# Optimization experiments

Hardware: AMD Instinct MI355X
Metric: run time of the kernel (lower is better)

Reference implementation:

```python
import jax, jax.numpy as jnp
import numpy as np

N = 8192
IN_F = 512
OUT_F = 256
ALPHA = 0.2          # LeakyReLU negative slope
MASK_VAL = -9e15     # same sentinel as the torch code


def setup_inputs() -> dict:
    key = jax.random.key(0)
    k1, k2, k3, k4, k5, k6 = jax.random.split(key, 6)
    inputs = jax.random.normal(k1, (N, IN_F), dtype=jnp.float32)
    # sparse-ish 0/1 dense adjacency (~avg degree 64)
    adj = (jax.random.uniform(k2, (N, N)) < (64.0 / N)).astype(jnp.float32)
    W = jax.random.normal(k3, (IN_F, OUT_F), dtype=jnp.float32) * (1.414 / np.sqrt(IN_F))
    a = jax.random.normal(k4, (2 * OUT_F, 1), dtype=jnp.float32) * 0.1
    W_gc = jax.random.normal(k5, (IN_F, OUT_F), dtype=jnp.float32) * (1.414 / np.sqrt(IN_F))
    b_gc = jax.random.normal(k6, (OUT_F,), dtype=jnp.float32) * 0.01
    return {"inputs": inputs, "adj": adj, "W": W, "a": a, "W_gc": W_gc, "b_gc": b_gc}


def reference(inputs, adj, W, a, W_gc, b_gc):
    # h: [n, F]
    h = inputs @ W
    F = h.shape[1]
    # Fused additive attention: e[i,j] = leaky_relu(a1.h_i + a2.h_j)
    # (mathematically identical to the repeat/cat construction in the source)
    f_src = h @ a[:F, 0]   # [n]
    f_dst = h @ a[F:, 0]   # [n]
    e = jax.nn.leaky_relu(f_src[:, None] + f_dst[None, :], negative_slope=ALPHA)  # [n, n]
    # masked row-softmax over neighbors
    att = jnp.where(adj > 0, e, MASK_VAL)
    att = jax.nn.softmax(att, axis=1)
    # dropout p=0.0 -> identity
    h_prime = att @ h  # [n, F]
    # optional dense graph-convolution branch (graph_convolve=True)
    gc = adj @ (inputs @ W_gc) + b_gc
    return h_prime + gc
```

## Files before the change

kernel.cpp:

```cpp
#include <hip/hip_runtime.h>
#include <hip/hip_bf16.h>
#include <math.h>

#define N_NODES 8192
#define IN_F    512
#define OUT_F   256
#define NCAT    512
#define ALPHA   0.2f
#define MAXDEG  512

typedef __attribute__((ext_vector_type(8))) short short8;
typedef __attribute__((ext_vector_type(4))) float f32x4;

static __device__ __forceinline__ short f2bf(float f) {
    union { float f; unsigned u; } v; v.f = f;
    unsigned r = v.u + 0x7fffu + ((v.u >> 16) & 1u);
    return (short)(r >> 16);
}
static __device__ __forceinline__ float bf2f(short s) {
    union { unsigned u; float f; } v;
    v.u = ((unsigned)(unsigned short)s) << 16;
    return v.f;
}

__global__ __launch_bounds__(512) void bt_pack(const float* __restrict__ W,
                                               const float* __restrict__ W_gc,
                                               short* __restrict__ Bt) {
    const int n = blockIdx.x;
    const int k = threadIdx.x;
    const int c = n >> 1;
    float v = (n & 1) ? W_gc[(size_t)k * OUT_F + c] : W[(size_t)k * OUT_F + c];
    Bt[(size_t)n * IN_F + k] = f2bf(v);
}

__global__ __launch_bounds__(256) void gemm_mfma(const float* __restrict__ A,
                                                 const short* __restrict__ Bt,
                                                 short* __restrict__ hcat) {
    __shared__ short As[128 * 32];
    __shared__ short Bs[128 * 32];

    const int tid  = threadIdx.x;
    const int m0   = blockIdx.y * 128;
    const int n0   = blockIdx.x * 128;
    const int wid  = tid >> 6;
    const int lane = tid & 63;
    const int wr   = wid >> 1;
    const int wc   = wid & 1;
    const int mh   = lane & 15;
    const int q    = lane >> 4;

    const int srow  = tid >> 1;
    const int shalf = tid & 1;

    const f32x4 vzero = {0.f, 0.f, 0.f, 0.f};
    f32x4 acc[4][4];
    #pragma unroll
    for (int i = 0; i < 4; i++)
        #pragma unroll
        for (int j = 0; j < 4; j++) acc[i][j] = vzero;

    const float* aga = A  + (size_t)(m0 + srow) * IN_F + shalf * 16;
    const short* bgb = Bt + (size_t)(n0 + srow) * IN_F + shalf * 16;
    short* asw = &As[srow * 32 + shalf * 16];
    short* bsw = &Bs[srow * 32 + shalf * 16];

    for (int k0 = 0; k0 < IN_F; k0 += 32) {
        const float4* a4 = (const float4*)(aga + k0);
        float4 x0 = a4[0], x1 = a4[1], x2 = a4[2], x3 = a4[3];
        const int4* b4 = (const int4*)(bgb + k0);
        int4 bv0 = b4[0], bv1 = b4[1];

        short8 p0, p1;
        p0[0] = f2bf(x0.x); p0[1] = f2bf(x0.y); p0[2] = f2bf(x0.z); p0[3] = f2bf(x0.w);
        p0[4] = f2bf(x1.x); p0[5] = f2bf(x1.y); p0[6] = f2bf(x1.z); p0[7] = f2bf(x1.w);
        p1[0] = f2bf(x2.x); p1[1] = f2bf(x2.y); p1[2] = f2bf(x2.z); p1[3] = f2bf(x2.w);
        p1[4] = f2bf(x3.x); p1[5] = f2bf(x3.y); p1[6] = f2bf(x3.z); p1[7] = f2bf(x3.w);

        __syncthreads();
        *(short8*)asw       = p0;
        *(short8*)(asw + 8) = p1;
        *(int4*)bsw         = bv0;
        *(int4*)(bsw + 8)   = bv1;
        __syncthreads();

        short8 af[4], bfm[4];
        #pragma unroll
        for (int i = 0; i < 4; i++) {
            af[i]  = *(const short8*)&As[(wr * 64 + i * 16 + mh) * 32 + q * 8];
            bfm[i] = *(const short8*)&Bs[(wc * 64 + i * 16 + mh) * 32 + q * 8];
        }
        #pragma unroll
        for (int mi = 0; mi < 4; mi++)
            #pragma unroll
            for (int ni = 0; ni < 4; ni++)
                acc[mi][ni] = __builtin_amdgcn_mfma_f32_16x16x32_bf16(
                    af[mi], bfm[ni], acc[mi][ni], 0, 0, 0);
    }

    #pragma unroll
    for (int mi = 0; mi < 4; mi++)
        #pragma unroll
        for (int ni = 0; ni < 4; ni++) {
            const int col   = n0 + wc * 64 + ni * 16 + mh;
            const int rbase = m0 + wr * 64 + mi * 16 + q * 4;
            f32x4 v = acc[mi][ni];
            #pragma unroll
            for (int r = 0; r < 4; r++)
                hcat[(size_t)(rbase + r) * NCAT + col] = f2bf(v[r]);
        }
}

__global__ __launch_bounds__(256) void compute_f(const short* __restrict__ hcat,
                                                 const float* __restrict__ a,
                                                 float* __restrict__ f_src,
                                                 float* __restrict__ f_dst) {
    const int row  = blockIdx.x * 4 + (threadIdx.x >> 6);
    const int lane = threadIdx.x & 63;
    const short* hr = hcat + (size_t)row * NCAT;
    float s1 = 0.f, s2 = 0.f;
    #pragma unroll
    for (int c = lane; c < OUT_F; c += 64) {
        float hv = bf2f(hr[2 * c]);
        s1 += hv * a[c];
        s2 += hv * a[OUT_F + c];
    }
    #pragma unroll
    for (int off = 32; off; off >>= 1) {
        s1 += __shfl_down(s1, off);
        s2 += __shfl_down(s2, off);
    }
    if (lane == 0) { f_src[row] = s1; f_dst[row] = s2; }
}

__global__ __launch_bounds__(256) void attn_row(const float* __restrict__ adj,
                                                const short* __restrict__ hcat,
                                                const float* __restrict__ f_src,
                                                const float* __restrict__ f_dst,
                                                const float* __restrict__ b_gc,
                                                float* __restrict__ out) {
    __shared__ int   s_idx[MAXDEG];
    __shared__ float s_w[MAXDEG];
    __shared__ float s_red[4];
    __shared__ int   s_count;

    const int row  = blockIdx.x;
    const int tid  = threadIdx.x;
    const int lane = tid & 63;
    const int wid  = tid >> 6;

    if (tid == 0) s_count = 0;
    __syncthreads();

    const float fs = f_src[row];
    const f32x4* arow4 = (const f32x4*)(adj + (size_t)row * N_NODES);

    f32x4 v[8];
    #pragma unroll
    for (int it = 0; it < 8; it++)
        v[it] = arow4[it * 256 + tid];

    float lloc = 0.f;
    #pragma unroll
    for (int it = 0; it < 8; it++) {
        int c4 = (v[it][0] > 0.f) + (v[it][1] > 0.f) +
                 (v[it][2] > 0.f) + (v[it][3] > 0.f);
        if (c4) {
            int pos = atomicAdd(&s_count, c4);
            const int j0 = (it * 256 + tid) * 4;
            #pragma unroll
            for (int i = 0; i < 4; i++) {
                if (v[it][i] > 0.f) {
                    float e = fs + f_dst[j0 + i];
                    e = (e > 0.f) ? e : ALPHA * e;
                    float w = __expf(e);
                    s_idx[pos] = j0 + i;
                    s_w[pos]   = w;
                    pos++;
                    lloc += w;
                }
            }
        }
    }
    #pragma unroll
    for (int off = 32; off; off >>= 1) lloc += __shfl_down(lloc, off);
    if (lane == 0) s_red[wid] = lloc;
    __syncthreads();

    const int   deg   = min(s_count, MAXDEG);
    const float l     = s_red[0] + s_red[1] + s_red[2] + s_red[3];
    const float inv_l = (deg > 0) ? 1.f / l : 0.f;

    const int u = lane >> 4;
    const int p = lane & 15;
    const short* hbase = hcat + wid * 128 + p * 8;

    float aa0 = 0.f, aa1 = 0.f, aa2 = 0.f, aa3 = 0.f;
    float gg0 = 0.f, gg1 = 0.f, gg2 = 0.f, gg3 = 0.f;
    #pragma unroll 4
    for (int k = u; k < deg; k += 4) {
        const int   j = s_idx[k];
        const float w = s_w[k];
        short8 hv = *(const short8*)(hbase + (size_t)j * NCAT);
        aa0 += w * bf2f(hv[0]); gg0 += bf2f(hv[1]);
        aa1 += w * bf2f(hv[2]); gg1 += bf2f(hv[3]);
        aa2 += w * bf2f(hv[4]); gg2 += bf2f(hv[5]);
        aa3 += w * bf2f(hv[6]); gg3 += bf2f(hv[7]);
    }
    aa0 += __shfl_down(aa0, 32); aa1 += __shfl_down(aa1, 32);
    aa2 += __shfl_down(aa2, 32); aa3 += __shfl_down(aa3, 32);
    gg0 += __shfl_down(gg0, 32); gg1 += __shfl_down(gg1, 32);
    gg2 += __shfl_down(gg2, 32); gg3 += __shfl_down(gg3, 32);
    aa0 += __shfl_down(aa0, 16); aa1 += __shfl_down(aa1, 16);
    aa2 += __shfl_down(aa2, 16); aa3 += __shfl_down(aa3, 16);
    gg0 += __shfl_down(gg0, 16); gg1 += __shfl_down(gg1, 16);
    gg2 += __shfl_down(gg2, 16); gg3 += __shfl_down(gg3, 16);

    if (u == 0) {
        const int col = wid * 64 + p * 4;
        const float4 bg = *(const float4*)(b_gc + col);
        float4 o;
        o.x = aa0 * inv_l + gg0 + bg.x;
        o.y = aa1 * inv_l + gg1 + bg.y;
        o.z = aa2 * inv_l + gg2 + bg.z;
        o.w = aa3 * inv_l + gg3 + bg.w;
        *(float4*)(out + (size_t)row * OUT_F + col) = o;
    }
}

extern "C" void kernel_launch(void* const* d_in, const int* in_sizes, int n_in,
                              void* d_out, int out_size, void* d_ws, size_t ws_size,
                              hipStream_t stream) {
    const float* inputs = (const float*)d_in[0];
    const float* adj    = (const float*)d_in[1];
    const float* W      = (const float*)d_in[2];
    const float* a      = (const float*)d_in[3];
    const float* W_gc   = (const float*)d_in[4];
    const float* b_gc   = (const float*)d_in[5];
    float* out = (float*)d_out;

    short* Bt    = (short*)d_ws;
    short* hcat  = Bt + (size_t)NCAT * IN_F;
    float* f_src = (float*)(hcat + (size_t)N_NODES * NCAT);
    float* f_dst = f_src + N_NODES;

    bt_pack<<<dim3(NCAT), dim3(IN_F), 0, stream>>>(W, W_gc, Bt);
    gemm_mfma<<<dim3(NCAT / 128, N_NODES / 128), 256, 0, stream>>>(inputs, Bt, hcat);
    compute_f<<<N_NODES / 4, 256, 0, stream>>>(hcat, a, f_src, f_dst);
    attn_row<<<N_NODES, 256, 0, stream>>>(adj, hcat, f_src, f_dst, b_gc, out);
}
```

Before: 425.2 us.

## Store attention features as FP8 in a per-row packed gather layout

The GEMM epilogue now writes the attention branch of h as software-encoded FP8 e4m3 alongside bf16 graph-conv features, in a 768-byte row layout. It also writes a separate bf16 copy of h for computing the attention logits. The attention gather therefore reads fewer bytes per neighbour, with each wave handling its own neighbours and a shared-memory reduction at the end. The cost is lower precision in the attention aggregation, a larger GEMM epilogue with an extra write, and added decode ALU work.

```diff
diff --git a/kernel.cpp b/kernel.cpp
--- a/kernel.cpp
+++ b/kernel.cpp
@@ -8,8 +8,10 @@
 #define NCAT    512
 #define ALPHA   0.2f
 #define MAXDEG  512
+#define RSTRIDE 768
 
 typedef __attribute__((ext_vector_type(8))) short short8;
+typedef __attribute__((ext_vector_type(4))) short short4e;
 typedef __attribute__((ext_vector_type(4))) float f32x4;
 
 static __device__ __forceinline__ short f2bf(float f) {
@@ -21,6 +23,35 @@
     union { unsigned u; float f; } v;
     v.u = ((unsigned)(unsigned short)s) << 16;
     return v.f;
+}
+
+static __device__ __forceinline__ unsigned char f2fp8(float f) {
+    union { float f; unsigned u; } v; v.f = f;
+    unsigned s = (v.u >> 24) & 0x80u;
+    float af = fabsf(f);
+    if (af >= 448.f) return (unsigned char)(s | 0x7Eu);
+    if (af < 0.015625f) {
+        int m = (int)rintf(af * 512.f);
+        if (m >= 8) return (unsigned char)(s | 0x08u);
+        return (unsigned char)(s | (unsigned)m);
+    }
+    unsigned u = v.u & 0x7FFFFFFFu;
+    unsigned t = u + 0x000FFFFFu + ((u >> 20) & 1u);
+    int e = (int)(t >> 23) - 127;
+    unsigned m3 = (t >> 20) & 7u;
+    if (e < -6) {
+        int m = (int)rintf(af * 512.f);
+        if (m >= 8) return (unsigned char)(s | 0x08u);
+        return (unsigned char)(s | (unsigned)m);
+    }
+    if (e > 8 || (e == 8 && m3 == 7u)) return (unsigned char)(s | 0x7Eu);
+    return (unsigned char)(s | (((unsigned)(e + 7)) << 3) | m3);
+}
+
+static __device__ __forceinline__ float fp8tof(unsigned b) {
+    union { unsigned u; float f; } v;
+    v.u = ((b & 0x80u) << 24) | ((b & 0x7Fu) << 20);
+    return v.f * 0x1p120f;
 }
 
 __global__ __launch_bounds__(512) void bt_pack(const float* __restrict__ W,
@@ -28,14 +59,15 @@
                                                short* __restrict__ Bt) {
     const int n = blockIdx.x;
     const int k = threadIdx.x;
-    const int c = n >> 1;
-    float v = (n & 1) ? W_gc[(size_t)k * OUT_F + c] : W[(size_t)k * OUT_F + c];
+    float v = (n < OUT_F) ? W[(size_t)k * OUT_F + n]
+                          : W_gc[(size_t)k * OUT_F + (n - OUT_F)];
     Bt[(size_t)n * IN_F + k] = f2bf(v);
 }
 
 __global__ __launch_bounds__(256) void gemm_mfma(const float* __restrict__ A,
                                                  const short* __restrict__ Bt,
-                                                 short* __restrict__ hcat) {
+                                                 unsigned char* __restrict__ hrow,
+                                                 short* __restrict__ hbf) {
     __shared__ short As[128 * 32];
     __shared__ short Bs[128 * 32];
 
@@ -97,32 +129,51 @@
                     af[mi], bfm[ni], acc[mi][ni], 0, 0, 0);
     }
 
-    #pragma unroll
-    for (int mi = 0; mi < 4; mi++)
-        #pragma unroll
-        for (int ni = 0; ni < 4; ni++) {
-            const int col   = n0 + wc * 64 + ni * 16 + mh;
-            const int rbase = m0 + wr * 64 + mi * 16 + q * 4;
-            f32x4 v = acc[mi][ni];
-            #pragma unroll
-            for (int r = 0; r < 4; r++)
-                hcat[(size_t)(rbase + r) * NCAT + col] = f2bf(v[r]);
-        }
-}
-
-__global__ __launch_bounds__(256) void compute_f(const short* __restrict__ hcat,
+    if (n0 < OUT_F) {
+        #pragma unroll
+        for (int mi = 0; mi < 4; mi++)
+            #pragma unroll
+            for (int ni = 0; ni < 4; ni++) {
+                const int col   = n0 + wc * 64 + ni * 16 + mh;
+                const int rbase = m0 + wr * 64 + mi * 16 + q * 4;
+                f32x4 v = acc[mi][ni];
+                #pragma unroll
+                for (int r = 0; r < 4; r++) {
+                    float x = v[r];
+                    hbf[(size_t)(rbase + r) * OUT_F + col] = f2bf(x);
+                    hrow[(size_t)(rbase + r) * RSTRIDE + col] = f2fp8(x);
+                }
+            }
+    } else {
+        #pragma unroll
+        for (int mi = 0; mi < 4; mi++)
+            #pragma unroll
+            for (int ni = 0; ni < 4; ni++) {
+                const int col   = (n0 - OUT_F) + wc * 64 + ni * 16 + mh;
+                const int rbase = m0 + wr * 64 + mi * 16 + q * 4;
+                f32x4 v = acc[mi][ni];
+                #pragma unroll
+                for (int r = 0; r < 4; r++)
+                    *(short*)(hrow + (size_t)(rbase + r) * RSTRIDE + 256 + 2 * col)
+                        = f2bf(v[r]);
+            }
+    }
+}
+
+__global__ __launch_bounds__(256) void compute_f(const short* __restrict__ hbf,
                                                  const float* __restrict__ a,
                                                  float* __restrict__ f_src,
                                                  float* __restrict__ f_dst) {
     const int row  = blockIdx.x * 4 + (threadIdx.x >> 6);
     const int lane = threadIdx.x & 63;
-    const short* hr = hcat + (size_t)row * NCAT;
+    const int c0   = lane * 4;
+    short4e v = *(const short4e*)(hbf + (size_t)row * OUT_F + c0);
     float s1 = 0.f, s2 = 0.f;
     #pragma unroll
-    for (int c = lane; c < OUT_F; c += 64) {
-        float hv = bf2f(hr[2 * c]);
-        s1 += hv * a[c];
-        s2 += hv * a[OUT_F + c];
+    for (int i = 0; i < 4; i++) {
+        float hv = bf2f(v[i]);
+        s1 += hv * a[c0 + i];
+        s2 += hv * a[OUT_F + c0 + i];
     }
     #pragma unroll
     for (int off = 32; off; off >>= 1) {
@@ -133,7 +184,7 @@
 }
 
 __global__ __launch_bounds__(256) void attn_row(const float* __restrict__ adj,
-                                                const short* __restrict__ hcat,
+                                                const unsigned char* __restrict__ hrow,
                                                 const float* __restrict__ f_src,
                                                 const float* __restrict__ f_dst,
                                                 const float* __restrict__ b_gc,
@@ -142,6 +193,7 @@
     __shared__ float s_w[MAXDEG];
     __shared__ float s_red[4];
     __shared__ int   s_count;
+    __shared__ float s_part[4][64][9];
 
     const int row  = blockIdx.x;
     const int tid  = threadIdx.x;
@@ -190,41 +242,37 @@
     const float l     = s_red[0] + s_red[1] + s_red[2] + s_red[3];
     const float inv_l = (deg > 0) ? 1.f / l : 0.f;
 
-    const int u = lane >> 4;
-    const int p = lane & 15;
-    const short* hbase = hcat + wid * 128 + p * 8;
-
-    float aa0 = 0.f, aa1 = 0.f, aa2 = 0.f, aa3 = 0.f;
-    float gg0 = 0.f, gg1 = 0.f, gg2 = 0.f, gg3 = 0.f;
+    const unsigned char* hb = hrow + lane * 4;
+    const unsigned char* gb = hrow + 256 + lane * 8;
+
+    float ah[4] = {0.f, 0.f, 0.f, 0.f};
+    float ag[4] = {0.f, 0.f, 0.f, 0.f};
     #pragma unroll 4
-    for (int k = u; k < deg; k += 4) {
-        const int   j = s_idx[k];
-        const float w = s_w[k];
-        short8 hv = *(const short8*)(hbase + (size_t)j * NCAT);
-        aa0 += w * bf2f(hv[0]); gg0 += bf2f(hv[1]);
-        aa1 += w * bf2f(hv[2]); gg1 += bf2f(hv[3]);
-        aa2 += w * bf2f(hv[4]); gg2 += bf2f(hv[5]);
-        aa3 += w * bf2f(hv[6]); gg3 += bf2f(hv[7]);
-    }
-    aa0 += __shfl_down(aa0, 32); aa1 += __shfl_down(aa1, 32);
-    aa2 += __shfl_down(aa2, 32); aa3 += __shfl_down(aa3, 32);
-    gg0 += __shfl_down(gg0, 32); gg1 += __shfl_down(gg1, 32);
-    gg2 += __shfl_down(gg2, 32); gg3 += __shfl_down(gg3, 32);
-    aa0 += __shfl_down(aa0, 16); aa1 += __shfl_down(aa1, 16);
-    aa2 += __shfl_down(aa2, 16); aa3 += __shfl_down(aa3, 16);
-    gg0 += __shfl_down(gg0, 16); gg1 += __shfl_down(gg1, 16);
-    gg2 += __shfl_down(gg2, 16); gg3 += __shfl_down(gg3, 16);
-
-    if (u == 0) {
-        const int col = wid * 64 + p * 4;
-        const float4 bg = *(const float4*)(b_gc + col);
-        float4 o;
-        o.x = aa0 * inv_l + gg0 + bg.x;
-        o.y = aa1 * inv_l + gg1 + bg.y;
-        o.z = aa2 * inv_l + gg2 + bg.z;
-        o.w = aa3 * inv_l + gg3 + bg.w;
-        *(float4*)(out + (size_t)row * OUT_F + col) = o;
-    }
+    for (int k = wid; k < deg; k += 4) {
+        const size_t off = (size_t)s_idx[k] * RSTRIDE;
+        const float  w   = s_w[k];
+        unsigned hp = *(const unsigned*)(hb + off);
+        short4e  gp = *(const short4e*)(gb + off);
+        ah[0] += w * fp8tof(hp & 0xFFu);
+        ah[1] += w * fp8tof((hp >> 8) & 0xFFu);
+        ah[2] += w * fp8tof((hp >> 16) & 0xFFu);
+        ah[3] += w * fp8tof(hp >> 24);
+        #pragma unroll
+        for (int i = 0; i < 4; i++) ag[i] += bf2f(gp[i]);
+    }
+    #pragma unroll
+    for (int i = 0; i < 4; i++) {
+        s_part[wid][lane][i]     = ah[i];
+        s_part[wid][lane][4 + i] = ag[i];
+    }
+    __syncthreads();
+
+    const int pc = tid >> 2, ic = tid & 3;
+    float h_tot = s_part[0][pc][ic]     + s_part[1][pc][ic]
+                + s_part[2][pc][ic]     + s_part[3][pc][ic];
+    float g_tot = s_part[0][pc][4 + ic] + s_part[1][pc][4 + ic]
+                + s_part[2][pc][4 + ic] + s_part[3][pc][4 + ic];
+    out[(size_t)row * OUT_F + tid] = h_tot * inv_l + g_tot + b_gc[tid];
 }
 
 extern "C" void kernel_launch(void* const* d_in, const int* in_sizes, int n_in,
@@ -238,13 +286,14 @@
     const float* b_gc   = (const float*)d_in[5];
     float* out = (float*)d_out;
 
-    short* Bt    = (short*)d_ws;
-    short* hcat  = Bt + (size_t)NCAT * IN_F;
-    float* f_src = (float*)(hcat + (size_t)N_NODES * NCAT);
-    float* f_dst = f_src + N_NODES;
+    short*         Bt    = (short*)d_ws;
+    unsigned char* hrow  = (unsigned char*)(Bt + (size_t)NCAT * IN_F);
+    short*         hbf   = (short*)(hrow + (size_t)N_NODES * RSTRIDE);
+    float*         f_src = (float*)(hbf + (size_t)N_NODES * OUT_F);
+    float*         f_dst = f_src + N_NODES;
 
     bt_pack<<<dim3(NCAT), dim3(IN_F), 0, stream>>>(W, W_gc, Bt);
-    gemm_mfma<<<dim3(NCAT / 128, N_NODES / 128), 256, 0, stream>>>(inputs, Bt, hcat);
-    compute_f<<<N_NODES / 4, 256, 0, stream>>>(hcat, a, f_src, f_dst);
-    attn_row<<<N_NODES, 256, 0, stream>>>(adj, hcat, f_src, f_dst, b_gc, out);
-}
+    gemm_mfma<<<dim3(NCAT / 128, N_NODES / 128), 256, 0, stream>>>(inputs, Bt, hrow, hbf);
+    compute_f<<<N_NODES / 4, 256, 0, stream>>>(hbf, a, f_src, f_dst);
+    attn_row<<<N_NODES, 256, 0, stream>>>(adj, hrow, f_src, f_dst, b_gc, out);
+}
```

Result: slower. 434.8 us (+2.3%).
